# Kernel tuning notes

Hardware: AMD Instinct MI355X
Metric: run time of the kernel (lower is better)

## Reference

```python
import jax, jax.numpy as jnp
import numpy as np

N = 100000   # total nodes in batched graph
E = 320000   # total edges
B = 128      # number of graphs in batch
D_IN = 128
H = 256
OUT = 10
L = 4        # num_layers - 1 conv layers
EPS = 1e-6


def setup_inputs() -> dict:
    key = jax.random.key(0)
    ks = jax.random.split(key, 8)
    h = jax.random.normal(ks[0], (N, D_IN), dtype=jnp.float32)
    src = jax.random.randint(ks[1], (E,), 0, N)
    dst = jax.random.randint(ks[2], (E,), 0, N)
    batch_ids = jnp.sort(jax.random.randint(ks[3], (N,), 0, B))
    s = 0.05
    W_first = jax.random.normal(ks[4], (D_IN, H), dtype=jnp.float32) * s
    b_first = jnp.zeros((H,), jnp.float32)
    W_rest = jax.random.normal(ks[5], (L - 1, H, H), dtype=jnp.float32) * s
    b_rest = jnp.zeros((L - 1, H), jnp.float32)
    gamma = jnp.ones((L, H), jnp.float32)
    beta = jnp.zeros((L, H), jnp.float32)
    mean_scale = jnp.ones((L, H), jnp.float32)
    W_pred = jax.random.normal(ks[6], (H, OUT), dtype=jnp.float32) * s
    b_pred = jnp.zeros((OUT,), jnp.float32)
    return dict(h=h, src=src, dst=dst, batch_ids=batch_ids,
                W_first=W_first, b_first=b_first, W_rest=W_rest, b_rest=b_rest,
                gamma=gamma, beta=beta, mean_scale=mean_scale,
                W_pred=W_pred, b_pred=b_pred)


def _graph_conv(h, W, b, src, dst, dinv_src, dinv_dst):
    # DGL GraphConv, norm='both': D_dst^{-1/2} A D_src^{-1/2} h W + b
    x = h * dinv_src[:, None]
    m = jax.ops.segment_sum(x[src], dst, num_segments=N)
    m = m * dinv_dst[:, None]
    return m @ W + b


def _graph_norm(h, gamma, beta, ms, batch_ids, counts):
    # GraphNorm: per-graph mean (scaled by learnable mean_scale) and std
    mean = jax.ops.segment_sum(h, batch_ids, num_segments=B) / counts[:, None]
    sub = h - mean[batch_ids] * ms
    var = jax.ops.segment_sum(sub * sub, batch_ids, num_segments=B) / counts[:, None]
    inv_std = jax.lax.rsqrt(var + EPS)
    return gamma * sub * inv_std[batch_ids] + beta


def reference(h, src, dst, batch_ids, W_first, b_first, W_rest, b_rest,
              gamma, beta, mean_scale, W_pred, b_pred):
    ones_e = jnp.ones((E,), h.dtype)
    deg_out = jnp.maximum(jax.ops.segment_sum(ones_e, src, num_segments=N), 1.0)
    deg_in = jnp.maximum(jax.ops.segment_sum(ones_e, dst, num_segments=N), 1.0)
    dinv_src = jax.lax.rsqrt(deg_out)
    dinv_dst = jax.lax.rsqrt(deg_in)
    counts = jnp.maximum(
        jax.ops.segment_sum(jnp.ones((N,), h.dtype), batch_ids, num_segments=B), 1.0)

    for i in range(L):
        x = h
        if i == 0:
            h = _graph_conv(h, W_first, b_first, src, dst, dinv_src, dinv_dst)
        else:
            h = _graph_conv(h, W_rest[i - 1], b_rest[i - 1], src, dst, dinv_src, dinv_dst)
        h = _graph_norm(h, gamma[i], beta[i], mean_scale[i], batch_ids, counts)
        if i != 0:
            h = jax.nn.relu(h) + x
        else:
            h = jax.nn.relu(h)

    pooled = jax.ops.segment_sum(h, batch_ids, num_segments=B)  # [B, H]
    # dropout is identity at eval
    return pooled @ W_pred + b_pred
```

## Files before the change

kernel.cpp:

```cpp
#include <hip/hip_runtime.h>

#define N_NODES 100000
#define N_PAD   100096
#define N_EDGES 320000
#define NB      128
#define DIN     128
#define H       256
#define OUT_DIM 10
#define EPSV    1e-6f
#define SCAN_B  256
#define PSLICES 32

typedef unsigned short bf16_t;
typedef __attribute__((ext_vector_type(8))) short bf16x8;
typedef __attribute__((ext_vector_type(4))) float f32x4;

__device__ __forceinline__ float bf2f(bf16_t u) {
    union { unsigned int i; float f; } x;
    x.i = ((unsigned int)u) << 16;
    return x.f;
}
__device__ __forceinline__ bf16_t f2bf(float f) {
    union { float f; unsigned int i; } x;
    x.f = f;
    unsigned int r = x.i + 0x7fffu + ((x.i >> 16) & 1u);
    return (bf16_t)(r >> 16);
}

__global__ void k_edge_deg(const int* __restrict__ src, const int* __restrict__ dst,
                           int* deg_out, int* deg_in) {
    int e = blockIdx.x * blockDim.x + threadIdx.x;
    if (e < N_EDGES) {
        atomicAdd(&deg_out[src[e]], 1);
        atomicAdd(&deg_in[dst[e]], 1);
    }
}

__global__ void k_dinv(const int* __restrict__ deg_out, const int* __restrict__ deg_in,
                       float* dinv_src, float* dinv_dst) {
    int n = blockIdx.x * blockDim.x + threadIdx.x;
    if (n < N_NODES) {
        dinv_src[n] = rsqrtf((float)max(deg_out[n], 1));
        dinv_dst[n] = rsqrtf((float)max(deg_in[n], 1));
    }
}

__global__ void k_gstart(const int* __restrict__ bid, int* __restrict__ gstart,
                         float* __restrict__ countsf) {
    int b = threadIdx.x;
    if (b <= NB) {
        int lo = 0, hi = N_NODES;
        while (lo < hi) {
            int mid = (lo + hi) >> 1;
            if (bid[mid] < b) lo = mid + 1; else hi = mid;
        }
        gstart[b] = lo;
    }
    __syncthreads();
    if (b < NB) countsf[b] = (float)max(gstart[b + 1] - gstart[b], 1);
}

__global__ void k_scan1(const int* __restrict__ deg, int* incl, int* bsums) {
    __shared__ int s[SCAN_B];
    int i = blockIdx.x * SCAN_B + threadIdx.x;
    int v = (i < N_NODES) ? deg[i] : 0;
    s[threadIdx.x] = v;
    __syncthreads();
    for (int d = 1; d < SCAN_B; d <<= 1) {
        int t = (threadIdx.x >= d) ? s[threadIdx.x - d] : 0;
        __syncthreads();
        s[threadIdx.x] += t;
        __syncthreads();
    }
    if (i < N_NODES) incl[i] = s[threadIdx.x];
    if (threadIdx.x == SCAN_B - 1) bsums[blockIdx.x] = s[threadIdx.x];
}

__global__ void k_scan2(const int* __restrict__ bsums, int* boffs, int nb) {
    __shared__ int s[512];
    int t = threadIdx.x;
    int v = (t < nb) ? bsums[t] : 0;
    s[t] = v;
    __syncthreads();
    for (int d = 1; d < 512; d <<= 1) {
        int x = (t >= d) ? s[t - d] : 0;
        __syncthreads();
        s[t] += x;
        __syncthreads();
    }
    if (t < nb) boffs[t] = s[t] - v;
}

__global__ void k_scan3(const int* __restrict__ deg, const int* __restrict__ incl,
                        const int* __restrict__ boffs, int* row_start, int* cursor) {
    int i = blockIdx.x * blockDim.x + threadIdx.x;
    if (i < N_NODES) {
        int ex = incl[i] - deg[i] + boffs[i / SCAN_B];
        row_start[i] = ex;
        cursor[i]    = ex;
    }
    if (i == 0) row_start[N_NODES] = N_EDGES;
}

__global__ void k_scatter(const int* __restrict__ src, const int* __restrict__ dst,
                          int* cursor, int* csr_src) {
    int e = blockIdx.x * blockDim.x + threadIdx.x;
    if (e < N_EDGES) {
        int slot = atomicAdd(&cursor[dst[e]], 1);
        csr_src[slot] = src[e];
    }
}

__global__ void k_wt_first(const float* __restrict__ W, bf16_t* __restrict__ Wt) {
    int idx = blockIdx.x * 256 + threadIdx.x;
    if (idx >= H * DIN) return;
    int c = idx / DIN, k = idx % DIN;
    Wt[idx] = f2bf(W[k * H + c]);
}
__global__ void k_wt_rest(const float* __restrict__ W, bf16_t* __restrict__ Wt) {
    int idx = blockIdx.x * 256 + threadIdx.x;
    if (idx >= 3 * H * H) return;
    int l = idx / (H * H);
    int rem = idx % (H * H);
    int c = rem / H, k = rem % H;
    Wt[idx] = f2bf(W[(size_t)l * H * H + k * H + c]);
}

__global__ void k_prescale(const float* __restrict__ h, const float* __restrict__ dinv_s,
                           bf16_t* __restrict__ hs) {
    int idx = blockIdx.x * blockDim.x + threadIdx.x;
    if (idx >= N_NODES * (DIN / 4)) return;
    int n = idx >> 5;
    float w = dinv_s[n];
    float4 v = reinterpret_cast<const float4*>(h)[idx];
    ushort4 o;
    o.x = f2bf(v.x * w); o.y = f2bf(v.y * w);
    o.z = f2bf(v.z * w); o.w = f2bf(v.w * w);
    reinterpret_cast<ushort4*>(hs)[idx] = o;
}

template <int NC, bool PS>
__global__ void k_agg(const bf16_t* __restrict__ hx, const float* __restrict__ dinv_s,
                      const float* __restrict__ dinv_d, const int* __restrict__ row_start,
                      const int* __restrict__ csr_src, bf16_t* __restrict__ m) {
    constexpr int VEC = NC / 64;
    int gid  = blockIdx.x * blockDim.x + threadIdx.x;
    int v    = gid >> 6;
    int lane = gid & 63;
    if (v >= N_NODES) return;
    float acc[VEC] = {};
    int s0 = row_start[v], s1 = row_start[v + 1];

    auto body = [&](int ei) {
        int si = csr_src[ei];
        float wv = 1.f;
        if constexpr (!PS) wv = dinv_s[si];
        if constexpr (VEC == 4) {
            ushort4 r = *reinterpret_cast<const ushort4*>(hx + (size_t)si * NC + lane * 4);
            acc[0] += bf2f(r.x) * wv; acc[1] += bf2f(r.y) * wv;
            acc[2] += bf2f(r.z) * wv; acc[3] += bf2f(r.w) * wv;
        } else {
            ushort2 r = *reinterpret_cast<const ushort2*>(hx + (size_t)si * NC + lane * 2);
            acc[0] += bf2f(r.x) * wv; acc[1] += bf2f(r.y) * wv;
        }
    };

    int e = s0;
    for (; e + 3 < s1; e += 4) { body(e); body(e + 1); body(e + 2); body(e + 3); }
    for (; e < s1; ++e) body(e);

    float wd = dinv_d[v];
    if constexpr (VEC == 4) {
        ushort4 o;
        o.x = f2bf(acc[0] * wd); o.y = f2bf(acc[1] * wd);
        o.z = f2bf(acc[2] * wd); o.w = f2bf(acc[3] * wd);
        *reinterpret_cast<ushort4*>(m + (size_t)v * NC + lane * 4) = o;
    } else {
        ushort2 o; o.x = f2bf(acc[0] * wd); o.y = f2bf(acc[1] * wd);
        *reinterpret_cast<ushort2*>(m + (size_t)v * NC + lane * 2) = o;
    }
}

template <int K>
__global__ __launch_bounds__(256) void k_gemm_mfma(const bf16_t* __restrict__ A,
                                                   const bf16_t* __restrict__ Wt,
                                                   const float* __restrict__ bias,
                                                   const int* __restrict__ bid,
                                                   bf16_t* __restrict__ C,
                                                   float* __restrict__ gsum,
                                                   float* __restrict__ gsumsq) {
    __shared__ bf16_t lds_raw[64 * (H + 8)];
    __shared__ int bid_lds[64];
    constexpr int LKA = K + 8;
    bf16_t (*aT)[LKA] = reinterpret_cast<bf16_t (*)[LKA]>(lds_raw);
    bf16_t (*cT)[H + 8] = reinterpret_cast<bf16_t (*)[H + 8]>(lds_raw);

    const int tid  = threadIdx.x;
    const int wave = tid >> 6;
    const int lane = tid & 63;
    const int row0 = blockIdx.x * 64;
    const int col0 = wave * 64;
    const int lr = lane & 15;
    const int lg = lane >> 4;

    {
        const bf16_t* Ag = A + (size_t)row0 * K;
        constexpr int CHUNKS = 64 * K / 8;
        #pragma unroll
        for (int it = 0; it < CHUNKS / 256; ++it) {
            int ci  = it * 256 + tid;
            int row = (ci * 8) / K;
            int col = (ci * 8) % K;
            uint4 v = *reinterpret_cast<const uint4*>(Ag + ci * 8);
            *reinterpret_cast<uint4*>(&aT[row][col]) = v;
        }
    }
    if (tid < 64) {
        int r = row0 + tid;
        bid_lds[tid] = (r < N_NODES) ? bid[r] : -1;
    }
    __syncthreads();

    f32x4 acc[4][4] = {};

    const bf16_t* Bb = Wt + (size_t)(col0 + lr) * K + lg * 8;

    #pragma unroll
    for (int ks = 0; ks < K / 32; ++ks) {
        bf16x8 a[4], b[4];
        #pragma unroll
        for (int mt = 0; mt < 4; ++mt)
            a[mt] = *reinterpret_cast<const bf16x8*>(&aT[mt * 16 + lr][ks * 32 + lg * 8]);
        #pragma unroll
        for (int nt = 0; nt < 4; ++nt)
            b[nt] = *reinterpret_cast<const bf16x8*>(Bb + (size_t)nt * 16 * K + ks * 32);
        #pragma unroll
        for (int mt = 0; mt < 4; ++mt)
            #pragma unroll
            for (int nt = 0; nt < 4; ++nt)
                acc[mt][nt] = __builtin_amdgcn_mfma_f32_16x16x32_bf16(a[mt], b[nt], acc[mt][nt], 0, 0, 0);
    }

    __syncthreads();

    #pragma unroll
    for (int nt = 0; nt < 4; ++nt) {
        int c = col0 + nt * 16 + lr;
        float bs = bias[c];
        #pragma unroll
        for (int mt = 0; mt < 4; ++mt) {
            #pragma unroll
            for (int j = 0; j < 4; ++j)
                cT[mt * 16 + lg * 4 + j][c] = f2bf(acc[mt][nt][j] + bs);
        }
    }
    __syncthreads();

    #pragma unroll
    for (int it = 0; it < 8; ++it) {
        int i = it * 256 + tid;
        int r = i >> 5;
        int s = i & 31;
        *reinterpret_cast<uint4*>(C + (size_t)(row0 + r) * H + s * 8) =
            *reinterpret_cast<const uint4*>(&cT[r][s * 8]);
    }

    {
        const int c = tid;
        float s = 0.f, q = 0.f;
        int gprev = bid_lds[0];
        #pragma unroll 8
        for (int r = 0; r < 64; ++r) {
            int g = bid_lds[r];
            if (g < 0) break;
            if (g != gprev) {
                atomicAdd(&gsum[gprev * H + c], s);
                atomicAdd(&gsumsq[gprev * H + c], q);
                s = 0.f; q = 0.f; gprev = g;
            }
            float v = bf2f(cT[r][c]);
            s += v; q += v * v;
        }
        if (gprev >= 0) {
            atomicAdd(&gsum[gprev * H + c], s);
            atomicAdd(&gsumsq[gprev * H + c], q);
        }
    }
}

__global__ void k_scaleshift(const float* __restrict__ countsf, const float* __restrict__ gamma,
                             const float* __restrict__ beta, const float* __restrict__ ms,
                             float* gsum, float* gsumsq) {
    int idx = blockIdx.x * blockDim.x + threadIdx.x;
    if (idx >= NB * H) return;
    int b = idx >> 8, f = idx & 255;
    float cnt  = countsf[b];
    float mean = gsum[idx] / cnt;
    float ex2  = gsumsq[idx] / cnt;
    float mm   = mean * ms[f];
    float var  = ex2 - 2.f * mean * mm + mm * mm;
    float rstd = rsqrtf(var + EPSV);
    float a    = gamma[f] * rstd;
    gsum[idx]   = a;
    gsumsq[idx] = beta[f] - a * mm;
}

template <bool RES>
__global__ void k_norm(const bf16_t* __restrict__ y, const bf16_t* __restrict__ resid,
                       const int* __restrict__ bid, const float* __restrict__ scale,
                       const float* __restrict__ shift, bf16_t* __restrict__ outp) {
    int idx = blockIdx.x * blockDim.x + threadIdx.x;
    if (idx >= N_NODES * (H / 4)) return;
    int n  = idx >> 6;
    int f4 = idx & 63;
    int b  = bid[n];
    ushort4 yv = reinterpret_cast<const ushort4*>(y)[idx];
    float4 sc = reinterpret_cast<const float4*>(scale)[b * 64 + f4];
    float4 sh = reinterpret_cast<const float4*>(shift)[b * 64 + f4];
    float o0 = fmaxf(bf2f(yv.x) * sc.x + sh.x, 0.f);
    float o1 = fmaxf(bf2f(yv.y) * sc.y + sh.y, 0.f);
    float o2 = fmaxf(bf2f(yv.z) * sc.z + sh.z, 0.f);
    float o3 = fmaxf(bf2f(yv.w) * sc.w + sh.w, 0.f);
    if constexpr (RES) {
        ushort4 r = reinterpret_cast<const ushort4*>(resid)[idx];
        o0 += bf2f(r.x); o1 += bf2f(r.y); o2 += bf2f(r.z); o3 += bf2f(r.w);
    }
    ushort4 o;
    o.x = f2bf(o0); o.y = f2bf(o1); o.z = f2bf(o2); o.w = f2bf(o3);
    reinterpret_cast<ushort4*>(outp)[idx] = o;
}

__global__ void k_pool(const bf16_t* __restrict__ hf, const int* __restrict__ gstart,
                       float* pooled) {
    int b = blockIdx.x, sl = blockIdx.y, f = threadIdx.x;
    int n0 = gstart[b], n1 = gstart[b + 1];
    int cnt = n1 - n0;
    int lo = n0 + (int)((long long)cnt * sl / PSLICES);
    int hi = n0 + (int)((long long)cnt * (sl + 1) / PSLICES);
    if (lo >= hi) return;
    float s = 0.f;
    for (int n = lo; n < hi; ++n) s += bf2f(hf[(size_t)n * H + f]);
    atomicAdd(&pooled[b * H + f], s);
}

__global__ void k_pred(const float* __restrict__ pooled, const float* __restrict__ Wp,
                       const float* __restrict__ bp, float* __restrict__ outp) {
    __shared__ float row[H];
    int b = blockIdx.x;
    row[threadIdx.x] = pooled[b * H + threadIdx.x];
    __syncthreads();
    if (threadIdx.x < OUT_DIM) {
        float acc = bp[threadIdx.x];
        for (int f = 0; f < H; ++f) acc += row[f] * Wp[f * OUT_DIM + threadIdx.x];
        outp[b * OUT_DIM + threadIdx.x] = acc;
    }
}

extern "C" void kernel_launch(void* const* d_in, const int* in_sizes, int n_in,
                              void* d_out, int out_size, void* d_ws, size_t ws_size,
                              hipStream_t stream) {
    const float* h_in  = (const float*)d_in[0];
    const int*   src   = (const int*)d_in[1];
    const int*   dst   = (const int*)d_in[2];
    const int*   bid   = (const int*)d_in[3];
    const float* Wf    = (const float*)d_in[4];
    const float* bfv   = (const float*)d_in[5];
    const float* Wr    = (const float*)d_in[6];
    const float* br    = (const float*)d_in[7];
    const float* gamma = (const float*)d_in[8];
    const float* beta  = (const float*)d_in[9];
    const float* ms    = (const float*)d_in[10];
    const float* Wp    = (const float*)d_in[11];
    const float* bp    = (const float*)d_in[12];
    float* outp = (float*)d_out;

    char* w = (char*)d_ws;
    size_t off = 0;
    auto alloc = [&](size_t bytes) -> void* {
        void* p = w + off;
        off = (off + bytes + 255) & ~(size_t)255;
        return p;
    };
    bf16_t* bufA = (bf16_t*)alloc((size_t)N_PAD * H * 2);
    bf16_t* bufB = (bf16_t*)alloc((size_t)N_PAD * H * 2);
    bf16_t* bufC = (bf16_t*)alloc((size_t)N_PAD * H * 2);
    bf16_t* Wt0  = (bf16_t*)alloc((size_t)H * DIN * 2);
    bf16_t* Wt123= (bf16_t*)alloc((size_t)3 * H * H * 2);
    int* deg_out_i = (int*)alloc(N_NODES * 4);
    int* deg_in_i  = (int*)alloc(N_NODES * 4);
    float* dinv_src = (float*)alloc(N_NODES * 4);
    float* dinv_dst = (float*)alloc(N_NODES * 4);
    int* incl_tmp  = (int*)alloc(N_NODES * 4);
    int* bsums     = (int*)alloc(512 * 4);
    int* boffs     = (int*)alloc(512 * 4);
    int* row_start = (int*)alloc((N_NODES + 1) * 4);
    int* cursor    = (int*)alloc(N_NODES * 4);
    int* csr_src   = (int*)alloc(N_EDGES * 4);
    int* gstart    = (int*)alloc((NB + 1) * 4);
    float* countsf = (float*)alloc(NB * 4);
    float* gsum    = (float*)alloc(NB * H * 4);
    float* gsumsq  = (float*)alloc(NB * H * 4);
    float* pooled  = (float*)alloc(NB * H * 4);

    if (off > ws_size) return;

    bf16_t* hs = bufB;

    const int nscan = (N_NODES + SCAN_B - 1) / SCAN_B;

    hipMemsetAsync(deg_out_i, 0, N_NODES * 4, stream);
    hipMemsetAsync(deg_in_i, 0, N_NODES * 4, stream);

    k_edge_deg<<<(N_EDGES + 255) / 256, 256, 0, stream>>>(src, dst, deg_out_i, deg_in_i);
    k_gstart<<<1, 256, 0, stream>>>(bid, gstart, countsf);
    k_dinv<<<(N_NODES + 255) / 256, 256, 0, stream>>>(deg_out_i, deg_in_i, dinv_src, dinv_dst);
    k_scan1<<<nscan, SCAN_B, 0, stream>>>(deg_in_i, incl_tmp, bsums);
    k_scan2<<<1, 512, 0, stream>>>(bsums, boffs, nscan);
    k_scan3<<<(N_NODES + 255) / 256, 256, 0, stream>>>(deg_in_i, incl_tmp, boffs, row_start, cursor);
    k_scatter<<<(N_EDGES + 255) / 256, 256, 0, stream>>>(src, dst, cursor, csr_src);
    k_wt_first<<<(H * DIN + 255) / 256, 256, 0, stream>>>(Wf, Wt0);
    k_wt_rest<<<(3 * H * H + 255) / 256, 256, 0, stream>>>(Wr, Wt123);

    const int aggGrid  = (N_NODES + 3) / 4;
    const int normGrid = (N_NODES * (H / 4) + 255) / 256;
    const int gemmGrid = N_PAD / 64;

    k_prescale<<<(N_NODES * (DIN / 4) + 255) / 256, 256, 0, stream>>>(h_in, dinv_src, hs);
    k_agg<DIN, true><<<aggGrid, 256, 0, stream>>>(hs, nullptr, dinv_dst, row_start, csr_src, bufA);
    hipMemsetAsync(gsum, 0, NB * H * 4, stream);
    hipMemsetAsync(gsumsq, 0, NB * H * 4, stream);
    k_gemm_mfma<DIN><<<gemmGrid, 256, 0, stream>>>(bufA, Wt0, bfv, bid, bufB, gsum, gsumsq);
    k_scaleshift<<<(NB * H + 255) / 256, 256, 0, stream>>>(countsf, gamma, beta, ms, gsum, gsumsq);
    k_norm<false><<<normGrid, 256, 0, stream>>>(bufB, nullptr, bid, gsum, gsumsq, bufC);

    bf16_t* hx = bufC;
    bf16_t* f1 = bufA;
    bf16_t* f2 = bufB;
    for (int i = 1; i < 4; ++i) {
        k_agg<H, false><<<aggGrid, 256, 0, stream>>>(hx, dinv_src, dinv_dst, row_start, csr_src, f1);
        hipMemsetAsync(gsum, 0, NB * H * 4, stream);
        hipMemsetAsync(gsumsq, 0, NB * H * 4, stream);
        k_gemm_mfma<H><<<gemmGrid, 256, 0, stream>>>(f1, Wt123 + (size_t)(i - 1) * H * H,
                                                     br + (i - 1) * H, bid, f2, gsum, gsumsq);
        k_scaleshift<<<(NB * H + 255) / 256, 256, 0, stream>>>(countsf, gamma + i * H, beta + i * H,
                                                               ms + i * H, gsum, gsumsq);
        k_norm<true><<<normGrid, 256, 0, stream>>>(f2, hx, bid, gsum, gsumsq, f1);
        bf16_t* nh = f1; f1 = hx; hx = nh;
    }

    hipMemsetAsync(pooled, 0, NB * H * 4, stream);
    k_pool<<<dim3(NB, PSLICES), H, 0, stream>>>(hx, gstart, pooled);
    k_pred<<<NB, H, 0, stream>>>(pooled, Wp, bp, outp);
}
```

Baseline: 632.9 us.

## Fuse GraphNorm scale/shift into norm kernel, batch memsets, load GEMM A from global

Removes the k_scaleshift kernel and recomputes the per-graph mean, variance and rsqrt inside k_norm for each element. Allocates separate per-layer stat buffers so that all memsets can be issued once up front instead of inside the layer loop. The GEMM no longer stages A in LDS and instead loads fragments straight from global memory, which drops a barrier but gives up LDS reuse and coalescing of the A tile. This trims launch overhead, at the cost of redundant rsqrt math per node and possibly less efficient A loads.

```diff
diff --git a/kernel.cpp b/kernel.cpp
--- a/kernel.cpp
+++ b/kernel.cpp
@@ -189,11 +189,8 @@
                                                    bf16_t* __restrict__ C,
                                                    float* __restrict__ gsum,
                                                    float* __restrict__ gsumsq) {
-    __shared__ bf16_t lds_raw[64 * (H + 8)];
+    __shared__ bf16_t cT[64][H + 8];
     __shared__ int bid_lds[64];
-    constexpr int LKA = K + 8;
-    bf16_t (*aT)[LKA] = reinterpret_cast<bf16_t (*)[LKA]>(lds_raw);
-    bf16_t (*cT)[H + 8] = reinterpret_cast<bf16_t (*)[H + 8]>(lds_raw);
 
     const int tid  = threadIdx.x;
     const int wave = tid >> 6;
@@ -203,45 +200,31 @@
     const int lr = lane & 15;
     const int lg = lane >> 4;
 
-    {
-        const bf16_t* Ag = A + (size_t)row0 * K;
-        constexpr int CHUNKS = 64 * K / 8;
-        #pragma unroll
-        for (int it = 0; it < CHUNKS / 256; ++it) {
-            int ci  = it * 256 + tid;
-            int row = (ci * 8) / K;
-            int col = (ci * 8) % K;
-            uint4 v = *reinterpret_cast<const uint4*>(Ag + ci * 8);
-            *reinterpret_cast<uint4*>(&aT[row][col]) = v;
-        }
-    }
     if (tid < 64) {
         int r = row0 + tid;
         bid_lds[tid] = (r < N_NODES) ? bid[r] : -1;
     }
-    __syncthreads();
+
+    const bf16_t* Ar = A  + (size_t)(row0 + lr) * K + lg * 8;
+    const bf16_t* Br = Wt + (size_t)(col0 + lr) * K + lg * 8;
 
     f32x4 acc[4][4] = {};
-
-    const bf16_t* Bb = Wt + (size_t)(col0 + lr) * K + lg * 8;
 
     #pragma unroll
     for (int ks = 0; ks < K / 32; ++ks) {
         bf16x8 a[4], b[4];
         #pragma unroll
         for (int mt = 0; mt < 4; ++mt)
-            a[mt] = *reinterpret_cast<const bf16x8*>(&aT[mt * 16 + lr][ks * 32 + lg * 8]);
+            a[mt] = *reinterpret_cast<const bf16x8*>(Ar + (size_t)mt * 16 * K + ks * 32);
         #pragma unroll
         for (int nt = 0; nt < 4; ++nt)
-            b[nt] = *reinterpret_cast<const bf16x8*>(Bb + (size_t)nt * 16 * K + ks * 32);
+            b[nt] = *reinterpret_cast<const bf16x8*>(Br + (size_t)nt * 16 * K + ks * 32);
         #pragma unroll
         for (int mt = 0; mt < 4; ++mt)
             #pragma unroll
             for (int nt = 0; nt < 4; ++nt)
                 acc[mt][nt] = __builtin_amdgcn_mfma_f32_16x16x32_bf16(a[mt], b[nt], acc[mt][nt], 0, 0, 0);
     }
-
-    __syncthreads();
 
     #pragma unroll
     for (int nt = 0; nt < 4; ++nt) {
@@ -288,39 +271,36 @@
     }
 }
 
-__global__ void k_scaleshift(const float* __restrict__ countsf, const float* __restrict__ gamma,
-                             const float* __restrict__ beta, const float* __restrict__ ms,
-                             float* gsum, float* gsumsq) {
-    int idx = blockIdx.x * blockDim.x + threadIdx.x;
-    if (idx >= NB * H) return;
-    int b = idx >> 8, f = idx & 255;
-    float cnt  = countsf[b];
-    float mean = gsum[idx] / cnt;
-    float ex2  = gsumsq[idx] / cnt;
-    float mm   = mean * ms[f];
-    float var  = ex2 - 2.f * mean * mm + mm * mm;
-    float rstd = rsqrtf(var + EPSV);
-    float a    = gamma[f] * rstd;
-    gsum[idx]   = a;
-    gsumsq[idx] = beta[f] - a * mm;
-}
-
 template <bool RES>
 __global__ void k_norm(const bf16_t* __restrict__ y, const bf16_t* __restrict__ resid,
-                       const int* __restrict__ bid, const float* __restrict__ scale,
-                       const float* __restrict__ shift, bf16_t* __restrict__ outp) {
+                       const int* __restrict__ bid, const float* __restrict__ gsum,
+                       const float* __restrict__ gsumsq, const float* __restrict__ countsf,
+                       const float* __restrict__ gamma, const float* __restrict__ beta,
+                       const float* __restrict__ msc, bf16_t* __restrict__ outp) {
     int idx = blockIdx.x * blockDim.x + threadIdx.x;
     if (idx >= N_NODES * (H / 4)) return;
     int n  = idx >> 6;
     int f4 = idx & 63;
     int b  = bid[n];
+    float rc = 1.0f / countsf[b];
+    float4 s4  = reinterpret_cast<const float4*>(gsum)[b * 64 + f4];
+    float4 q4  = reinterpret_cast<const float4*>(gsumsq)[b * 64 + f4];
+    float4 g4  = reinterpret_cast<const float4*>(gamma)[f4];
+    float4 be4 = reinterpret_cast<const float4*>(beta)[f4];
+    float4 m4  = reinterpret_cast<const float4*>(msc)[f4];
     ushort4 yv = reinterpret_cast<const ushort4*>(y)[idx];
-    float4 sc = reinterpret_cast<const float4*>(scale)[b * 64 + f4];
-    float4 sh = reinterpret_cast<const float4*>(shift)[b * 64 + f4];
-    float o0 = fmaxf(bf2f(yv.x) * sc.x + sh.x, 0.f);
-    float o1 = fmaxf(bf2f(yv.y) * sc.y + sh.y, 0.f);
-    float o2 = fmaxf(bf2f(yv.z) * sc.z + sh.z, 0.f);
-    float o3 = fmaxf(bf2f(yv.w) * sc.w + sh.w, 0.f);
+
+    auto nrm = [&](float s, float q, float ga, float be, float m, float yy) {
+        float mean = s * rc, ex2 = q * rc;
+        float mm   = mean * m;
+        float var  = ex2 - 2.f * mean * mm + mm * mm;
+        float a    = ga * rsqrtf(var + EPSV);
+        return fmaxf(yy * a + (be - a * mm), 0.f);
+    };
+    float o0 = nrm(s4.x, q4.x, g4.x, be4.x, m4.x, bf2f(yv.x));
+    float o1 = nrm(s4.y, q4.y, g4.y, be4.y, m4.y, bf2f(yv.y));
+    float o2 = nrm(s4.z, q4.z, g4.z, be4.z, m4.z, bf2f(yv.z));
+    float o3 = nrm(s4.w, q4.w, g4.w, be4.w, m4.w, bf2f(yv.w));
     if constexpr (RES) {
         ushort4 r = reinterpret_cast<const ushort4*>(resid)[idx];
         o0 += bf2f(r.x); o1 += bf2f(r.y); o2 += bf2f(r.z); o3 += bf2f(r.w);
@@ -398,8 +378,8 @@
     int* csr_src   = (int*)alloc(N_EDGES * 4);
     int* gstart    = (int*)alloc((NB + 1) * 4);
     float* countsf = (float*)alloc(NB * 4);
-    float* gsum    = (float*)alloc(NB * H * 4);
-    float* gsumsq  = (float*)alloc(NB * H * 4);
+    float* gsum    = (float*)alloc((size_t)4 * NB * H * 4);
+    float* gsumsq  = (float*)alloc((size_t)4 * NB * H * 4);
     float* pooled  = (float*)alloc(NB * H * 4);
 
     if (off > ws_size) return;
@@ -410,6 +390,9 @@
 
     hipMemsetAsync(deg_out_i, 0, N_NODES * 4, stream);
     hipMemsetAsync(deg_in_i, 0, N_NODES * 4, stream);
+    hipMemsetAsync(gsum, 0, (size_t)4 * NB * H * 4, stream);
+    hipMemsetAsync(gsumsq, 0, (size_t)4 * NB * H * 4, stream);
+    hipMemsetAsync(pooled, 0, NB * H * 4, stream);
 
     k_edge_deg<<<(N_EDGES + 255) / 256, 256, 0, stream>>>(src, dst, deg_out_i, deg_in_i);
     k_gstart<<<1, 256, 0, stream>>>(bid, gstart, countsf);
@@ -427,28 +410,24 @@
 
     k_prescale<<<(N_NODES * (DIN / 4) + 255) / 256, 256, 0, stream>>>(h_in, dinv_src, hs);
     k_agg<DIN, true><<<aggGrid, 256, 0, stream>>>(hs, nullptr, dinv_dst, row_start, csr_src, bufA);
-    hipMemsetAsync(gsum, 0, NB * H * 4, stream);
-    hipMemsetAsync(gsumsq, 0, NB * H * 4, stream);
     k_gemm_mfma<DIN><<<gemmGrid, 256, 0, stream>>>(bufA, Wt0, bfv, bid, bufB, gsum, gsumsq);
-    k_scaleshift<<<(NB * H + 255) / 256, 256, 0, stream>>>(countsf, gamma, beta, ms, gsum, gsumsq);
-    k_norm<false><<<normGrid, 256, 0, stream>>>(bufB, nullptr, bid, gsum, gsumsq, bufC);
+    k_norm<false><<<normGrid, 256, 0, stream>>>(bufB, nullptr, bid, gsum, gsumsq, countsf,
+                                                gamma, beta, ms, bufC);
 
     bf16_t* hx = bufC;
     bf16_t* f1 = bufA;
     bf16_t* f2 = bufB;
     for (int i = 1; i < 4; ++i) {
+        float* gs = gsum   + (size_t)i * NB * H;
+        float* gq = gsumsq + (size_t)i * NB * H;
         k_agg<H, false><<<aggGrid, 256, 0, stream>>>(hx, dinv_src, dinv_dst, row_start, csr_src, f1);
-        hipMemsetAsync(gsum, 0, NB * H * 4, stream);
-        hipMemsetAsync(gsumsq, 0, NB * H * 4, stream);
         k_gemm_mfma<H><<<gemmGrid, 256, 0, stream>>>(f1, Wt123 + (size_t)(i - 1) * H * H,
-                                                     br + (i - 1) * H, bid, f2, gsum, gsumsq);
-        k_scaleshift<<<(NB * H + 255) / 256, 256, 0, stream>>>(countsf, gamma + i * H, beta + i * H,
-                                                               ms + i * H, gsum, gsumsq);
-        k_norm<true><<<normGrid, 256, 0, stream>>>(f2, hx, bid, gsum, gsumsq, f1);
+                                                     br + (i - 1) * H, bid, f2, gs, gq);
+        k_norm<true><<<normGrid, 256, 0, stream>>>(f2, hx, bid, gs, gq, countsf,
+                                                   gamma + i * H, beta + i * H, ms + i * H, f1);
         bf16_t* nh = f1; f1 = hx; hx = nh;
     }
 
-    hipMemsetAsync(pooled, 0, NB * H * 4, stream);
     k_pool<<<dim3(NB, PSLICES), H, 0, stream>>>(hx, gstart, pooled);
     k_pred<<<NB, H, 0, stream>>>(pooled, Wp, bp, outp);
 }
```

Measured after the change: 636.2 us. No clear change (+0.5%).
